# Kernel tuning notes

Hardware: AMD Instinct MI355X
Metric: run time of the kernel (lower is better)

## Reference

```python
import jax, jax.numpy as jnp
import numpy as np

N = 100_000      # nodes
F_IN = 256       # num_features
HID = 128        # args.hidden
C = 32           # num_classes
E = 1_600_000    # edges
EPS = 0.1        # AntiSymmetricConv epsilon
GAMMA = 0.1      # AntiSymmetricConv gamma


def setup_inputs() -> dict:
    key = jax.random.key(0)
    ks = jax.random.split(key, 10)
    def rn(k, shape, scale=0.05):
        return jax.random.normal(k, shape, dtype=jnp.float32) * scale
    x = jax.random.normal(ks[0], (N, F_IN), dtype=jnp.float32)
    edge_index = jax.random.randint(ks[1], (2, E), 0, N, dtype=jnp.int32)
    return {
        "x": x,
        "lin1_w": rn(ks[2], (HID, F_IN)), "lin1_b": jnp.zeros((HID,), jnp.float32),
        "lin2_w": rn(ks[3], (C, HID)),   "lin2_b": jnp.zeros((C,), jnp.float32),
        "W1": rn(ks[4], (HID, HID)), "phi1_w": rn(ks[5], (HID, HID)), "b1": jnp.zeros((HID,), jnp.float32),
        "W2": rn(ks[6], (C, C)),     "phi2_w": rn(ks[7], (C, C)),     "b2": jnp.zeros((C,), jnp.float32),
        "edge_index": edge_index,
    }


def gcn_norm(edge_index, n):
    # GCNConv default: add self-loops, symmetric D^-1/2 (A+I) D^-1/2 normalization
    loops = jnp.arange(n, dtype=edge_index.dtype)
    row = jnp.concatenate([edge_index[0], loops])  # source
    col = jnp.concatenate([edge_index[1], loops])  # target (aggregation)
    deg = jax.ops.segment_sum(jnp.ones(row.shape[0], jnp.float32), col, num_segments=n)
    dinv = jnp.where(deg > 0, jax.lax.rsqrt(deg), 0.0)
    return row, col, dinv[row] * dinv[col]


def gcn_conv(x, phi_w, row, col, norm):
    xw = x @ phi_w.T                                  # [N, d]
    msgs = norm[:, None] * xw[row]                    # [E+N, d] gather
    return jax.ops.segment_sum(msgs, col, num_segments=x.shape[0])  # scatter-add


def anti_symmetric_conv(x, row, col, norm, W, phi_w, b):
    d = W.shape[0]
    aw = W - W.T - GAMMA * jnp.eye(d, dtype=W.dtype)  # antisymmetric weight
    h = gcn_conv(x, phi_w, row, col, norm)            # phi(x, edge_index)
    h = jnp.tanh(x @ aw.T + h + b)
    return x + EPS * h                                # one Euler step (num_iters=1)


def reference(x, lin1_w, lin1_b, lin2_w, lin2_b, W1, phi1_w, b1, W2, phi2_w, b2, edge_index):
    row, col, norm = gcn_norm(edge_index, x.shape[0])
    h = jax.nn.relu(x @ lin1_w.T + lin1_b)            # dropout is identity in eval
    h = anti_symmetric_conv(h, row, col, norm, W1, phi1_w, b1)
    h = h @ lin2_w.T + lin2_b
    h = anti_symmetric_conv(h, row, col, norm, W2, phi2_w, b2)
    return jax.nn.log_softmax(h, axis=1)
```

## Files before the change

### kernel.cpp

```cpp
#include <hip/hip_runtime.h>
#include <hip/hip_bf16.h>
#include <math.h>

#define N_NODES 100000
#define F_IN    256
#define HID     128
#define NCLS    32
#define NEDGES  1600000
#define EPS_C   0.1f
#define GAMMA_C 0.1f

#define NBK   782
#define CHUNK 4096
#define NCH   391
#define BMAX  4096

typedef __attribute__((ext_vector_type(8))) short short8;
typedef __attribute__((ext_vector_type(4))) float floatx4;

__device__ __forceinline__ float bf2f(unsigned short u) {
    union { unsigned int u; float f; } c;
    c.u = ((unsigned int)u) << 16;
    return c.f;
}
__device__ __forceinline__ unsigned short f2bf(float f) {
    union { float f; unsigned int u; } c; c.f = f;
    unsigned int u = c.u;
    u += 0x7FFFu + ((u >> 16) & 1u);
    return (unsigned short)(u >> 16);
}

__device__ __forceinline__ short8 cvt8(float4 u, float4 v) {
    short8 r;
    r[0] = (short)f2bf(u.x); r[1] = (short)f2bf(u.y);
    r[2] = (short)f2bf(u.z); r[3] = (short)f2bf(u.w);
    r[4] = (short)f2bf(v.x); r[5] = (short)f2bf(v.y);
    r[6] = (short)f2bf(v.z); r[7] = (short)f2bf(v.w);
    return r;
}

__device__ __forceinline__ float ldf(const void* p, size_t i, int md) {
    return md ? ((const float*)p)[i] : bf2f(((const unsigned short*)p)[i]);
}

__global__ void k_detect(const unsigned short* __restrict__ x, int* __restrict__ mode) {
    __shared__ int cnt;
    if (threadIdx.x == 0) cnt = 0;
    __syncthreads();
    float v = fabsf(bf2f(x[2 * threadIdx.x]));
    if (v > 1e4f || !isfinite(v)) atomicAdd(&cnt, 1);
    __syncthreads();
    if (threadIdx.x == 0) *mode = (cnt >= 8) ? 1 : 0;
}

__global__ __launch_bounds__(256) void k_cvtx(const void* __restrict__ x,
                                              unsigned short* __restrict__ xbf,
                                              const int* __restrict__ dmode, int n8) {
    if (!dmode[0]) return;
    const float* xf = (const float*)x;
    int stride = gridDim.x * 256;
    for (int i = blockIdx.x * 256 + threadIdx.x; i < n8; i += stride) {
        const float* q = xf + (size_t)i * 8;
        float4 u = *(const float4*)q, v = *(const float4*)(q + 4);
        *(short8*)(xbf + (size_t)i * 8) = cvt8(u, v);
    }
}

__global__ __launch_bounds__(256) void k_cvtw(const void* __restrict__ w1,
                                              const void* __restrict__ w2,
                                              const void* __restrict__ w3,
                                              const void* __restrict__ w4,
                                              unsigned short* __restrict__ out,
                                              const int* __restrict__ dmode) {
    if (!dmode[0]) return;
    int i = blockIdx.x * 256 + threadIdx.x;
    const float* src; int off;
    if (i < 4096)      { src = (const float*)w1; off = i; }
    else if (i < 6144) { src = (const float*)w2; off = i - 4096; }
    else if (i < 6656) { src = (const float*)w3; off = i - 6144; }
    else if (i < 6784) { src = (const float*)w4; off = i - 6656; }
    else return;
    const float* q = src + (size_t)off * 8;
    *(short8*)(out + (size_t)i * 8) = cvt8(*(const float4*)q, *(const float4*)(q + 4));
}

__global__ __launch_bounds__(256) void k_hist2(const int* __restrict__ ecol,
                                               int* __restrict__ hist, int e) {
    __shared__ int lh[NBK];
    for (int i = threadIdx.x; i < NBK; i += 256) lh[i] = 0;
    __syncthreads();
    int base = blockIdx.x * CHUNK;
    int lim = base + CHUNK; if (lim > e) lim = e;
    for (int i = base + threadIdx.x; i < lim; i += 256)
        atomicAdd(&lh[ecol[i] >> 7], 1);
    __syncthreads();
    for (int i = threadIdx.x; i < NBK; i += 256) hist[blockIdx.x * NBK + i] = lh[i];
}

__global__ __launch_bounds__(256) void k_tot(const int* __restrict__ hist, int* __restrict__ tot) {
    __shared__ int s[256];
    int b = blockIdx.x;
    int v = 0;
    for (int blk = threadIdx.x; blk < NCH; blk += 256) v += hist[blk * NBK + b];
    s[threadIdx.x] = v;
    __syncthreads();
#pragma unroll
    for (int off = 128; off > 0; off >>= 1) {
        if (threadIdx.x < off) s[threadIdx.x] += s[threadIdx.x + off];
        __syncthreads();
    }
    if (threadIdx.x == 0) tot[b] = s[0];
}

__global__ void k_bscan(const int* __restrict__ tot, int* __restrict__ bbase) {
    __shared__ int s[1024];
    int v = (threadIdx.x < NBK) ? tot[threadIdx.x] : 0;
    s[threadIdx.x] = v;
    __syncthreads();
#pragma unroll
    for (int off = 1; off < 1024; off <<= 1) {
        int t = (threadIdx.x >= off) ? s[threadIdx.x - off] : 0;
        __syncthreads();
        s[threadIdx.x] += t;
        __syncthreads();
    }
    if (threadIdx.x < NBK) bbase[threadIdx.x] = s[threadIdx.x] - v;
}

__global__ __launch_bounds__(512) void k_colscan(const int* __restrict__ hist,
                                                 const int* __restrict__ bbase,
                                                 int* __restrict__ off) {
    __shared__ int s[512];
    int b = blockIdx.x, t = threadIdx.x;
    int v = (t < NCH) ? hist[t * NBK + b] : 0;
    s[t] = v;
    __syncthreads();
#pragma unroll
    for (int o = 1; o < 512; o <<= 1) {
        int u = (t >= o) ? s[t - o] : 0;
        __syncthreads();
        s[t] += u;
        __syncthreads();
    }
    if (t < NCH) off[t * NBK + b] = s[t] - v + bbase[b];
}

__global__ __launch_bounds__(256) void k_pass3(
    const int* __restrict__ erow, const int* __restrict__ ecol,
    const int* __restrict__ off, unsigned int* __restrict__ pairs, int e)
{
    __shared__ int lh[NBK];
    __shared__ int lex[NBK + 1];
    __shared__ int cur[NBK];
    __shared__ int wsum[256];
    __shared__ unsigned int sp[CHUNK];
    int base = blockIdx.x * CHUNK;
    int lim = base + CHUNK; if (lim > e) lim = e;
    int cnt = lim - base;

    for (int i = threadIdx.x; i < NBK; i += 256) lh[i] = 0;
    __syncthreads();
    for (int i = base + threadIdx.x; i < lim; i += 256)
        atomicAdd(&lh[ecol[i] >> 7], 1);
    __syncthreads();

    int t4 = threadIdx.x * 4;
    int a0 = (t4 + 0 < NBK) ? lh[t4 + 0] : 0;
    int a1 = (t4 + 1 < NBK) ? lh[t4 + 1] : 0;
    int a2 = (t4 + 2 < NBK) ? lh[t4 + 2] : 0;
    int a3 = (t4 + 3 < NBK) ? lh[t4 + 3] : 0;
    int mysum = a0 + a1 + a2 + a3;
    wsum[threadIdx.x] = mysum;
    __syncthreads();
#pragma unroll
    for (int o = 1; o < 256; o <<= 1) {
        int u = (threadIdx.x >= o) ? wsum[threadIdx.x - o] : 0;
        __syncthreads();
        wsum[threadIdx.x] += u;
        __syncthreads();
    }
    int run = wsum[threadIdx.x] - mysum;
    if (t4 + 0 < NBK) { lex[t4 + 0] = run;            cur[t4 + 0] = run; }
    if (t4 + 1 < NBK) { lex[t4 + 1] = run + a0;       cur[t4 + 1] = run + a0; }
    if (t4 + 2 < NBK) { lex[t4 + 2] = run + a0 + a1;  cur[t4 + 2] = run + a0 + a1; }
    if (t4 + 3 < NBK) { lex[t4 + 3] = run + a0 + a1 + a2; cur[t4 + 3] = run + a0 + a1 + a2; }
    if (threadIdx.x == 0) lex[NBK] = cnt;
    __syncthreads();

    for (int i = base + threadIdx.x; i < lim; i += 256) {
        int dst = ecol[i], src = erow[i];
        int b = dst >> 7;
        int p = atomicAdd(&cur[b], 1);
        sp[p] = ((unsigned int)src << 7) | (unsigned int)(dst & 127);
    }
    __syncthreads();

    for (int i = threadIdx.x; i < cnt; i += 256) {
        int loB = 0, hiB = NBK;
        while (hiB - loB > 1) {
            int mid = (loB + hiB) >> 1;
            if (lex[mid] <= i) loB = mid; else hiB = mid;
        }
        pairs[off[blockIdx.x * NBK + loB] + (i - lex[loB])] = sp[i];
    }
}

__global__ __launch_bounds__(256) void k_build(
    const int* __restrict__ tot, const int* __restrict__ bbase,
    const unsigned int* __restrict__ pairs,
    int* __restrict__ srt, int* __restrict__ row_start, int* __restrict__ cend,
    float* __restrict__ dinv, int n)
{
    __shared__ int lh[128];
    __shared__ int lo[128];
    __shared__ unsigned int se[BMAX];
    int b = blockIdx.x;
    int nb = tot[b]; if (nb > BMAX) nb = BMAX;
    int base = bbase[b];
    if (threadIdx.x < 128) lh[threadIdx.x] = 0;
    __syncthreads();
    for (int e = threadIdx.x; e < nb; e += 256) {
        unsigned int pk = pairs[(size_t)base + e];
        se[e] = pk;
        atomicAdd(&lh[pk & 127u], 1);
    }
    __syncthreads();
    if (threadIdx.x < 128) lo[threadIdx.x] = lh[threadIdx.x];
    __syncthreads();
#pragma unroll
    for (int off = 1; off < 128; off <<= 1) {
        int t = (threadIdx.x < 128 && threadIdx.x >= off) ? lo[threadIdx.x - off] : 0;
        __syncthreads();
        if (threadIdx.x < 128) lo[threadIdx.x] += t;
        __syncthreads();
    }
    int node = b * 128 + threadIdx.x;
    if (threadIdx.x < 128 && node < n) {
        int inc = lo[threadIdx.x], cnt = lh[threadIdx.x];
        row_start[node] = base + inc - cnt;
        cend[node]      = base + inc;
        dinv[node]      = rsqrtf((float)cnt + 1.0f);
    }
    __syncthreads();
    if (threadIdx.x < 128) lh[threadIdx.x] = lo[threadIdx.x] - lh[threadIdx.x];
    __syncthreads();
    for (int e = threadIdx.x; e < nb; e += 256) {
        unsigned int pk = se[e];
        int pos = atomicAdd(&lh[pk & 127u], 1);
        srt[base + pos] = (int)(pk >> 7);
    }
}

__global__ void k_aw(const void* __restrict__ W, unsigned short* __restrict__ aw,
                     const int* __restrict__ dmode, int d) {
    int idx = blockIdx.x * blockDim.x + threadIdx.x;
    if (idx >= d * d) return;
    int md = dmode[0];
    int n = idx / d, k = idx - n * d;
    float v = ldf(W, n * d + k, md) - ldf(W, k * d + n, md) - ((n == k) ? GAMMA_C : 0.0f);
    aw[idx] = f2bf(v);
}

template<int K, int NCB, int NCF, int EPI, int NSPLIT, bool ASEL, bool BSEL>
__global__ __launch_bounds__(512) void k_gemm6(
    const void* A, const unsigned short* Acvt,
    const void* B, const unsigned short* Bcvt, const void* bias,
    unsigned short* Cout,
    const unsigned short* agg, const unsigned short* xw, const float* dinv,
    const int* dmode, void* opout, int M)
{
    constexpr int KP = K + 8;
    constexpr int NT = NCB / 16;
    constexpr int KS = K / 32;
    constexpr int SN = (NCB * K) / 4096;
    __shared__ __align__(16) unsigned short sB[NCB * KP];
    const int md = dmode[0];

    const unsigned short* Ab = (ASEL && md) ? Acvt : (const unsigned short*)A;
    const unsigned short* Bb = (BSEL && md) ? Bcvt : (const unsigned short*)B;

    const int rowblk = (NSPLIT > 1) ? ((int)blockIdx.x / NSPLIT) : (int)blockIdx.x;
    const int col0   = (NSPLIT > 1) ? ((int)blockIdx.x % NSPLIT) * NCB : 0;

    const int lane = threadIdx.x & 63;
    const int wave = threadIdx.x >> 6;
    const int l15  = lane & 15;
    const int quad = lane >> 4;
    const int row0 = rowblk * 128 + wave * 16;

    int ar = row0 + l15;
    int am = ar < M ? ar : M - 1;

    short8 a[KS];
#pragma unroll
    for (int s = 0; s < KS; ++s)
        a[s] = *(const short8*)(Ab + (size_t)am * K + s * 32 + quad * 8);

    if constexpr (SN >= 1) {
        short8 st[SN];
#pragma unroll
        for (int i = 0; i < SN; ++i) {
            int base = threadIdx.x * 8 + i * 4096;
            int r = base / K, c = base % K;
            st[i] = *(const short8*)(Bb + (size_t)(col0 + r) * K + c);
        }
#pragma unroll
        for (int i = 0; i < SN; ++i) {
            int base = threadIdx.x * 8 + i * 4096;
            int r = base / K, c = base % K;
            *(short8*)(sB + r * KP + c) = st[i];
        }
    } else {
        if (threadIdx.x < (NCB * K) / 8) {
            int base = threadIdx.x * 8;
            int r = base / K, c = base % K;
            *(short8*)(sB + r * KP + c) =
                *(const short8*)(Bb + (size_t)(col0 + r) * K + c);
        }
    }
    __builtin_amdgcn_sched_barrier(0);
    __syncthreads();

    floatx4 acc[NT];
#pragma unroll
    for (int t = 0; t < NT; ++t) acc[t] = (floatx4){0.f, 0.f, 0.f, 0.f};

#pragma unroll
    for (int s = 0; s < KS; ++s) {
        short8 b[NT];
#pragma unroll
        for (int t = 0; t < NT; ++t)
            b[t] = *(const short8*)(sB + (t * 16 + l15) * KP + s * 32 + quad * 8);
#pragma unroll
        for (int t = 0; t < NT; ++t)
            acc[t] = __builtin_amdgcn_mfma_f32_16x16x32_bf16(a[s], b[t], acc[t], 0, 0, 0);
    }

    const unsigned short* Ares = Ab;
#pragma unroll
    for (int reg = 0; reg < 4; ++reg) {
        int rr = row0 + quad * 4 + reg;
        if (EPI == 4) {
            int rrc = rr < M ? rr : M - 1;
            float dv = dinv[rrc];
            float val[NT];
#pragma unroll
            for (int t = 0; t < NT; ++t) {
                int col = t * 16 + l15;
                float z = acc[t][reg]
                        + bf2f(agg[(size_t)rrc * NCF + col])
                        + dv * bf2f(xw[(size_t)rrc * NCF + col])
                        + ldf(bias, col, md);
                val[t] = bf2f(Ares[(size_t)rrc * K + col]) + EPS_C * tanhf(z);
            }
            float m = val[0];
#pragma unroll
            for (int t = 1; t < NT; ++t) m = fmaxf(m, val[t]);
#pragma unroll
            for (int msk = 1; msk < 16; msk <<= 1) m = fmaxf(m, __shfl_xor(m, msk));
            float s = 0.f;
#pragma unroll
            for (int t = 0; t < NT; ++t) s += expf(val[t] - m);
#pragma unroll
            for (int msk = 1; msk < 16; msk <<= 1) s += __shfl_xor(s, msk);
            float ls = m + logf(s);
            if (rr < M) {
#pragma unroll
                for (int t = 0; t < NT; ++t) {
                    int col = t * 16 + l15;
                    float r = val[t] - ls;
                    if (md) ((float*)opout)[(size_t)rr * NCF + col] = r;
                    else    ((unsigned short*)opout)[(size_t)rr * NCF + col] = f2bf(r);
                }
            }
        } else {
            if (rr >= M) continue;
#pragma unroll
            for (int t = 0; t < NT; ++t) {
                int gcol = col0 + t * 16 + l15;
                float v = acc[t][reg];
                if (EPI == 0) { v += ldf(bias, gcol, md); v = v > 0.f ? v : 0.f; }
                else if (EPI == 5) { v *= dinv[rr]; }
                else if (EPI == 3) {
                    float dv = dinv[rr];
                    float z = v + bf2f(agg[(size_t)rr * NCF + gcol])
                            + dv * bf2f(xw[(size_t)rr * NCF + gcol])
                            + ldf(bias, gcol, md);
                    v = bf2f(Ares[(size_t)rr * K + gcol]) + EPS_C * tanhf(z);
                }
                Cout[(size_t)rr * NCF + gcol] = f2bf(v);
            }
        }
    }
}

__global__ __launch_bounds__(256) void k_lin2phi2(
    const unsigned short* __restrict__ A,
    const void* __restrict__ B1, const unsigned short* __restrict__ B1c,
    const void* __restrict__ bias,
    const void* __restrict__ B2, const unsigned short* __restrict__ B2c,
    unsigned short* __restrict__ h3, unsigned short* __restrict__ xws2,
    const float* __restrict__ dinv, const int* __restrict__ dmode, int M)
{
    constexpr int K1 = 128, KP1 = 136, KP2 = 40;
    __shared__ __align__(16) unsigned short sB1[32 * KP1];
    __shared__ __align__(16) unsigned short sB2[32 * KP2];
    __shared__ __align__(16) unsigned short sT[128 * KP2];
    const int md = dmode[0];

    const unsigned short* B1b = md ? B1c : (const unsigned short*)B1;
    const unsigned short* B2b = md ? B2c : (const unsigned short*)B2;

    const int lane = threadIdx.x & 63;
    const int wave = threadIdx.x >> 6;
    const int l15  = lane & 15;
    const int quad = lane >> 4;
    const int row0 = blockIdx.x * 128 + wave * 32;

    int am[2];
#pragma unroll
    for (int rt = 0; rt < 2; ++rt) {
        int r = row0 + rt * 16 + l15;
        am[rt] = r < M ? r : M - 1;
    }

    short8 a1[4][2];
#pragma unroll
    for (int s = 0; s < 4; ++s)
#pragma unroll
        for (int rt = 0; rt < 2; ++rt)
            a1[s][rt] = *(const short8*)(A + (size_t)am[rt] * K1 + s * 32 + quad * 8);

    short8 s1[2], s2;
    const bool has2 = threadIdx.x * 8 < 1024;
#pragma unroll
    for (int i = 0; i < 2; ++i)
        s1[i] = *(const short8*)(B1b + threadIdx.x * 8 + i * 2048);
    if (has2)
        s2 = *(const short8*)(B2b + threadIdx.x * 8);
#pragma unroll
    for (int i = 0; i < 2; ++i) {
        int base = threadIdx.x * 8 + i * 2048;
        int r = base / K1, c = base - r * K1;
        *(short8*)(sB1 + r * KP1 + c) = s1[i];
    }
    if (has2) {
        int base = threadIdx.x * 8;
        int r = base / 32, c = base - r * 32;
        *(short8*)(sB2 + r * KP2 + c) = s2;
    }
    __builtin_amdgcn_sched_barrier(0);
    __syncthreads();

    floatx4 acc[2][2];
#pragma unroll
    for (int rt = 0; rt < 2; ++rt) { acc[rt][0] = (floatx4){0,0,0,0}; acc[rt][1] = (floatx4){0,0,0,0}; }

#pragma unroll
    for (int s = 0; s < 4; ++s) {
#pragma unroll
        for (int rt = 0; rt < 2; ++rt) {
#pragma unroll
            for (int t = 0; t < 2; ++t) {
                short8 b = *(const short8*)(sB1 + (t * 16 + l15) * KP1 + s * 32 + quad * 8);
                acc[rt][t] = __builtin_amdgcn_mfma_f32_16x16x32_bf16(a1[s][rt], b, acc[rt][t], 0, 0, 0);
            }
        }
    }
#pragma unroll
    for (int rt = 0; rt < 2; ++rt)
#pragma unroll
        for (int reg = 0; reg < 4; ++reg) {
            int rr = row0 + rt * 16 + quad * 4 + reg;
            int lr = wave * 32 + rt * 16 + quad * 4 + reg;
#pragma unroll
            for (int t = 0; t < 2; ++t) {
                int col = t * 16 + l15;
                unsigned short hv = f2bf(acc[rt][t][reg] + ldf(bias, col, md));
                sT[lr * KP2 + col] = hv;
                if (rr < M) h3[(size_t)rr * 32 + col] = hv;
            }
        }
    __syncthreads();

    floatx4 a2[2][2];
#pragma unroll
    for (int rt = 0; rt < 2; ++rt) {
        short8 a = *(const short8*)(sT + (wave * 32 + rt * 16 + l15) * KP2 + quad * 8);
#pragma unroll
        for (int t = 0; t < 2; ++t) {
            short8 b = *(const short8*)(sB2 + (t * 16 + l15) * KP2 + quad * 8);
            a2[rt][t] = __builtin_amdgcn_mfma_f32_16x16x32_bf16(a, b, (floatx4){0,0,0,0}, 0, 0, 0);
        }
    }
#pragma unroll
    for (int rt = 0; rt < 2; ++rt)
#pragma unroll
        for (int reg = 0; reg < 4; ++reg) {
            int rr = row0 + rt * 16 + quad * 4 + reg;
            if (rr >= M) continue;
            float dv = dinv[rr];
#pragma unroll
            for (int t = 0; t < 2; ++t)
                xws2[(size_t)rr * 32 + t * 16 + l15] = f2bf(dv * a2[rt][t][reg]);
        }
}

__global__ __launch_bounds__(256) void k_gather128(
    const int* __restrict__ srt, const int* __restrict__ rs,
    const int* __restrict__ cend,
    const unsigned short* __restrict__ xws, const float* __restrict__ dinv,
    unsigned short* __restrict__ agg, int n)
{
    int node = blockIdx.x * 8 + (threadIdx.x >> 5);
    int l = threadIdx.x & 31;
    if (node >= n) return;
    int j = rs[node], end = cend[node];
    float a0 = 0.f, a1 = 0.f, a2 = 0.f, a3 = 0.f;
    int jend = j + ((end - j) & ~7);
    while (j < jend) {
        int idx[8];
#pragma unroll
        for (int k = 0; k < 8; ++k) idx[k] = srt[j + k];
        uint2 p[8];
#pragma unroll
        for (int k = 0; k < 8; ++k)
            p[k] = *(const uint2*)(xws + (size_t)idx[k] * 128 + l * 4);
#pragma unroll
        for (int k = 0; k < 8; ++k) {
            a0 += bf2f((unsigned short)(p[k].x & 0xFFFFu));
            a1 += bf2f((unsigned short)(p[k].x >> 16));
            a2 += bf2f((unsigned short)(p[k].y & 0xFFFFu));
            a3 += bf2f((unsigned short)(p[k].y >> 16));
        }
        j += 8;
    }
    if (j < end) {
        int idx[8];
#pragma unroll
        for (int k = 0; k < 8; ++k) {
            int jj = j + k;
            idx[k] = srt[jj < end ? jj : end - 1];
        }
        uint2 p[8];
#pragma unroll
        for (int k = 0; k < 8; ++k)
            p[k] = *(const uint2*)(xws + (size_t)idx[k] * 128 + l * 4);
#pragma unroll
        for (int k = 0; k < 8; ++k) {
            if (j + k < end) {
                a0 += bf2f((unsigned short)(p[k].x & 0xFFFFu));
                a1 += bf2f((unsigned short)(p[k].x >> 16));
                a2 += bf2f((unsigned short)(p[k].y & 0xFFFFu));
                a3 += bf2f((unsigned short)(p[k].y >> 16));
            }
        }
    }
    float dn = dinv[node];
    uint2 out;
    out.x = (unsigned int)f2bf(dn * a0) | ((unsigned int)f2bf(dn * a1) << 16);
    out.y = (unsigned int)f2bf(dn * a2) | ((unsigned int)f2bf(dn * a3) << 16);
    *(uint2*)(agg + (size_t)node * 128 + l * 4) = out;
}

__global__ __launch_bounds__(256) void k_gather32(
    const int* __restrict__ srt, const int* __restrict__ rs,
    const int* __restrict__ cend,
    const unsigned short* __restrict__ xws, const float* __restrict__ dinv,
    unsigned short* __restrict__ agg, int n)
{
    int node = blockIdx.x * 32 + (threadIdx.x >> 3);
    int l = threadIdx.x & 7;
    if (node >= n) return;
    int j = rs[node], end = cend[node];
    float a0 = 0.f, a1 = 0.f, a2 = 0.f, a3 = 0.f;
    int jend = j + ((end - j) & ~7);
    while (j < jend) {
        int idx[8];
#pragma unroll
        for (int k = 0; k < 8; ++k) idx[k] = srt[j + k];
        uint2 p[8];
#pragma unroll
        for (int k = 0; k < 8; ++k)
            p[k] = *(const uint2*)(xws + (size_t)idx[k] * 32 + l * 4);
#pragma unroll
        for (int k = 0; k < 8; ++k) {
            a0 += bf2f((unsigned short)(p[k].x & 0xFFFFu));
            a1 += bf2f((unsigned short)(p[k].x >> 16));
            a2 += bf2f((unsigned short)(p[k].y & 0xFFFFu));
            a3 += bf2f((unsigned short)(p[k].y >> 16));
        }
        j += 8;
    }
    if (j < end) {
        int idx[8];
#pragma unroll
        for (int k = 0; k < 8; ++k) {
            int jj = j + k;
            idx[k] = srt[jj < end ? jj : end - 1];
        }
        uint2 p[8];
#pragma unroll
        for (int k = 0; k < 8; ++k)
            p[k] = *(const uint2*)(xws + (size_t)idx[k] * 32 + l * 4);
#pragma unroll
        for (int k = 0; k < 8; ++k) {
            if (j + k < end) {
                a0 += bf2f((unsigned short)(p[k].x & 0xFFFFu));
                a1 += bf2f((unsigned short)(p[k].x >> 16));
                a2 += bf2f((unsigned short)(p[k].y & 0xFFFFu));
                a3 += bf2f((unsigned short)(p[k].y >> 16));
            }
        }
    }
    float dn = dinv[node];
    uint2 out;
    out.x = (unsigned int)f2bf(dn * a0) | ((unsigned int)f2bf(dn * a1) << 16);
    out.y = (unsigned int)f2bf(dn * a2) | ((unsigned int)f2bf(dn * a3) << 16);
    *(uint2*)(agg + (size_t)node * 32 + l * 4) = out;
}

extern "C" void kernel_launch(void* const* d_in, const int* in_sizes, int n_in,
                              void* d_out, int out_size, void* d_ws, size_t ws_size,
                              hipStream_t stream)
{
    const void* x      = d_in[0];
    const void* lin1_w = d_in[1];
    const void* lin1_b = d_in[2];
    const void* lin2_w = d_in[3];
    const void* lin2_b = d_in[4];
    const void* W1     = d_in[5];
    const void* phi1w  = d_in[6];
    const void* b1     = d_in[7];
    const void* W2     = d_in[8];
    const void* phi2w  = d_in[9];
    const void* b2     = d_in[10];
    const int* eidx    = (const int*)d_in[11];
    const int* erow = eidx;
    const int* ecol = eidx + NEDGES;

    char* ws = (char*)d_ws;
    float* dinv          = (float*)ws;
    int*   dmode         = (int*)(ws + 400000);
    unsigned short* aw1  = (unsigned short*)(ws + 401408);
    unsigned short* aw2  = (unsigned short*)(ws + 435200);
    int* tot             = (int*)(ws + 440320);
    int* bbase           = (int*)(ws + 443648);
    int* row_start       = (int*)(ws + 446976);
    int* cend            = (int*)(ws + 846976);
    int* srt             = (int*)(ws + 1246976);
    int* hist            = (int*)(ws + 7646976);
    int* offb            = (int*)(ws + 8870912);
    unsigned short* wbf  = (unsigned short*)(ws + 10094080);
    unsigned short* h1   = (unsigned short*)(ws + 10485760);
    unsigned short* xws1 = h1 + (size_t)N_NODES * HID;
    unsigned short* agg1 = xws1 + (size_t)N_NODES * HID;
    unsigned short* h2   = xws1;
    unsigned short* h3   = h1;
    unsigned short* xws2 = agg1;
    unsigned short* agg2 = agg1 + (size_t)N_NODES * NCLS;
    unsigned int* pairs  = (unsigned int*)agg1;
    unsigned short* xbf  = xws1;

    unsigned short* bw1 = wbf;
    unsigned short* bp1 = wbf + 32768;
    unsigned short* bw2 = wbf + 49152;
    unsigned short* bp2 = wbf + 53248;

    const int GB = 256;
    const int NB5 = (N_NODES + 127) / 128;
    k_detect<<<1, 256, 0, stream>>>((const unsigned short*)x, dmode);

    k_hist2<<<NCH, 256, 0, stream>>>(ecol, hist, NEDGES);
    k_tot<<<NBK, 256, 0, stream>>>(hist, tot);
    k_bscan<<<1, 1024, 0, stream>>>(tot, bbase);
    k_colscan<<<NBK, 512, 0, stream>>>(hist, bbase, offb);
    k_pass3<<<NCH, 256, 0, stream>>>(erow, ecol, offb, pairs, NEDGES);
    k_build<<<NBK, 256, 0, stream>>>(tot, bbase, pairs, srt, row_start, cend, dinv, N_NODES);

    k_aw<<<(HID * HID + GB - 1) / GB, GB, 0, stream>>>(W1, aw1, dmode, HID);
    k_aw<<<(NCLS * NCLS + GB - 1) / GB, GB, 0, stream>>>(W2, aw2, dmode, NCLS);
    k_cvtw<<<27, 256, 0, stream>>>(lin1_w, phi1w, lin2_w, phi2w, wbf, dmode);
    k_cvtx<<<2048, 256, 0, stream>>>(x, xbf, dmode, N_NODES * F_IN / 8);

    k_gemm6<256, 64, 128, 0, 2, true, true><<<NB5 * 2, 512, 0, stream>>>(
        x, xbf, lin1_w, bw1, lin1_b, h1, nullptr, nullptr, nullptr, dmode, nullptr, N_NODES);
    k_gemm6<128, 128, 128, 5, 1, false, true><<<NB5, 512, 0, stream>>>(
        h1, nullptr, phi1w, bp1, nullptr, xws1, nullptr, nullptr, dinv, dmode, nullptr, N_NODES);
    k_gather128<<<(N_NODES + 7) / 8, 256, 0, stream>>>(
        srt, row_start, cend, xws1, dinv, agg1, N_NODES);
    k_gemm6<128, 128, 128, 3, 1, false, false><<<NB5, 512, 0, stream>>>(
        h1, nullptr, aw1, nullptr, b1, h2, agg1, xws1, dinv, dmode, nullptr, N_NODES);
    k_lin2phi2<<<(N_NODES + 127) / 128, 256, 0, stream>>>(
        h2, lin2_w, bw2, lin2_b, phi2w, bp2, h3, xws2, dinv, dmode, N_NODES);
    k_gather32<<<(N_NODES + 31) / 32, 256, 0, stream>>>(
        srt, row_start, cend, xws2, dinv, agg2, N_NODES);
    k_gemm6<32, 32, 32, 4, 1, false, false><<<NB5, 512, 0, stream>>>(
        h3, nullptr, aw2, nullptr, b2, nullptr, agg2, xws2, dinv, dmode, d_out, N_NODES);
}
```

Baseline: 427.9 us.

## Sort nodes by degree for gathers, widen gather loads, drop pass3 binary search

Adds a counting sort of nodes by in-degree (histogram, scan, scatter) so that gather kernels process nodes in degree order, which is meant to reduce wavefront divergence from unequal neighbor counts. The gather kernels now use 16-byte loads with 8 elements per lane, halving the lanes per node. k_pass3 stores each edge's bucket id in shared memory instead of binary-searching the bucket for every output element. The change adds four small kernel launches and an extra ord indirection, and output writes become scattered by node order.

```diff
diff --git a/kernel.cpp b/kernel.cpp
--- a/kernel.cpp
+++ b/kernel.cpp
@@ -150,10 +150,11 @@
     const int* __restrict__ off, unsigned int* __restrict__ pairs, int e)
 {
     __shared__ int lh[NBK];
-    __shared__ int lex[NBK + 1];
+    __shared__ int lex[NBK];
     __shared__ int cur[NBK];
     __shared__ int wsum[256];
     __shared__ unsigned int sp[CHUNK];
+    __shared__ unsigned short sbk[CHUNK];
     int base = blockIdx.x * CHUNK;
     int lim = base + CHUNK; if (lim > e) lim = e;
     int cnt = lim - base;
@@ -184,7 +185,6 @@
     if (t4 + 1 < NBK) { lex[t4 + 1] = run + a0;       cur[t4 + 1] = run + a0; }
     if (t4 + 2 < NBK) { lex[t4 + 2] = run + a0 + a1;  cur[t4 + 2] = run + a0 + a1; }
     if (t4 + 3 < NBK) { lex[t4 + 3] = run + a0 + a1 + a2; cur[t4 + 3] = run + a0 + a1 + a2; }
-    if (threadIdx.x == 0) lex[NBK] = cnt;
     __syncthreads();
 
     for (int i = base + threadIdx.x; i < lim; i += 256) {
@@ -192,16 +192,13 @@
         int b = dst >> 7;
         int p = atomicAdd(&cur[b], 1);
         sp[p] = ((unsigned int)src << 7) | (unsigned int)(dst & 127);
+        sbk[p] = (unsigned short)b;
     }
     __syncthreads();
 
     for (int i = threadIdx.x; i < cnt; i += 256) {
-        int loB = 0, hiB = NBK;
-        while (hiB - loB > 1) {
-            int mid = (loB + hiB) >> 1;
-            if (lex[mid] <= i) loB = mid; else hiB = mid;
-        }
-        pairs[off[blockIdx.x * NBK + loB] + (i - lex[loB])] = sp[i];
+        int b = sbk[i];
+        pairs[off[blockIdx.x * NBK + b] + (i - lex[b])] = sp[i];
     }
 }
 
@@ -248,6 +245,43 @@
         unsigned int pk = se[e];
         int pos = atomicAdd(&lh[pk & 127u], 1);
         srt[base + pos] = (int)(pk >> 7);
+    }
+}
+
+__global__ void k_dzero(int* __restrict__ dh) { dh[threadIdx.x] = 0; }
+
+__global__ __launch_bounds__(256) void k_dhist(const int* __restrict__ rs,
+                                               const int* __restrict__ ce,
+                                               int* __restrict__ dh, int n) {
+    __shared__ int lh[64];
+    if (threadIdx.x < 64) lh[threadIdx.x] = 0;
+    __syncthreads();
+    for (int i = blockIdx.x * 256 + threadIdx.x; i < n; i += gridDim.x * 256) {
+        int d = ce[i] - rs[i]; if (d > 63) d = 63;
+        atomicAdd(&lh[d], 1);
+    }
+    __syncthreads();
+    if (threadIdx.x < 64 && lh[threadIdx.x]) atomicAdd(&dh[threadIdx.x], lh[threadIdx.x]);
+}
+
+__global__ void k_dscan(const int* __restrict__ dh, int* __restrict__ dcur) {
+    __shared__ int s[64];
+    int v = dh[threadIdx.x]; s[threadIdx.x] = v; __syncthreads();
+#pragma unroll
+    for (int o = 1; o < 64; o <<= 1) {
+        int t = (threadIdx.x >= o) ? s[threadIdx.x - o] : 0;
+        __syncthreads(); s[threadIdx.x] += t; __syncthreads();
+    }
+    dcur[threadIdx.x] = s[threadIdx.x] - v;
+}
+
+__global__ __launch_bounds__(256) void k_dscat(const int* __restrict__ rs,
+                                               const int* __restrict__ ce,
+                                               int* __restrict__ dcur,
+                                               int* __restrict__ ord, int n) {
+    for (int i = blockIdx.x * 256 + threadIdx.x; i < n; i += gridDim.x * 256) {
+        int d = ce[i] - rs[i]; if (d > 63) d = 63;
+        ord[atomicAdd(&dcur[d], 1)] = i;
     }
 }
 
@@ -508,31 +542,30 @@
 
 __global__ __launch_bounds__(256) void k_gather128(
     const int* __restrict__ srt, const int* __restrict__ rs,
-    const int* __restrict__ cend,
+    const int* __restrict__ cend, const int* __restrict__ ord,
     const unsigned short* __restrict__ xws, const float* __restrict__ dinv,
     unsigned short* __restrict__ agg, int n)
 {
-    int node = blockIdx.x * 8 + (threadIdx.x >> 5);
-    int l = threadIdx.x & 31;
-    if (node >= n) return;
+    int gid = blockIdx.x * 16 + (threadIdx.x >> 4);
+    int l = threadIdx.x & 15;
+    if (gid >= n) return;
+    int node = ord[gid];
     int j = rs[node], end = cend[node];
-    float a0 = 0.f, a1 = 0.f, a2 = 0.f, a3 = 0.f;
+    float ac[8] = {0.f, 0.f, 0.f, 0.f, 0.f, 0.f, 0.f, 0.f};
     int jend = j + ((end - j) & ~7);
     while (j < jend) {
         int idx[8];
 #pragma unroll
         for (int k = 0; k < 8; ++k) idx[k] = srt[j + k];
-        uint2 p[8];
+        short8 p[8];
 #pragma unroll
         for (int k = 0; k < 8; ++k)
-            p[k] = *(const uint2*)(xws + (size_t)idx[k] * 128 + l * 4);
-#pragma unroll
-        for (int k = 0; k < 8; ++k) {
-            a0 += bf2f((unsigned short)(p[k].x & 0xFFFFu));
-            a1 += bf2f((unsigned short)(p[k].x >> 16));
-            a2 += bf2f((unsigned short)(p[k].y & 0xFFFFu));
-            a3 += bf2f((unsigned short)(p[k].y >> 16));
-        }
+            p[k] = *(const short8*)(xws + (size_t)idx[k] * 128 + l * 8);
+#pragma unroll
+        for (int k = 0; k < 8; ++k)
+#pragma unroll
+            for (int e = 0; e < 8; ++e)
+                ac[e] += bf2f((unsigned short)p[k][e]);
         j += 8;
     }
     if (j < end) {
@@ -542,54 +575,52 @@
             int jj = j + k;
             idx[k] = srt[jj < end ? jj : end - 1];
         }
-        uint2 p[8];
+        short8 p[8];
 #pragma unroll
         for (int k = 0; k < 8; ++k)
-            p[k] = *(const uint2*)(xws + (size_t)idx[k] * 128 + l * 4);
+            p[k] = *(const short8*)(xws + (size_t)idx[k] * 128 + l * 8);
 #pragma unroll
         for (int k = 0; k < 8; ++k) {
             if (j + k < end) {
-                a0 += bf2f((unsigned short)(p[k].x & 0xFFFFu));
-                a1 += bf2f((unsigned short)(p[k].x >> 16));
-                a2 += bf2f((unsigned short)(p[k].y & 0xFFFFu));
-                a3 += bf2f((unsigned short)(p[k].y >> 16));
+#pragma unroll
+                for (int e = 0; e < 8; ++e)
+                    ac[e] += bf2f((unsigned short)p[k][e]);
             }
         }
     }
     float dn = dinv[node];
-    uint2 out;
-    out.x = (unsigned int)f2bf(dn * a0) | ((unsigned int)f2bf(dn * a1) << 16);
-    out.y = (unsigned int)f2bf(dn * a2) | ((unsigned int)f2bf(dn * a3) << 16);
-    *(uint2*)(agg + (size_t)node * 128 + l * 4) = out;
+    short8 out;
+#pragma unroll
+    for (int e = 0; e < 8; ++e) out[e] = (short)f2bf(dn * ac[e]);
+    *(short8*)(agg + (size_t)node * 128 + l * 8) = out;
 }
 
 __global__ __launch_bounds__(256) void k_gather32(
     const int* __restrict__ srt, const int* __restrict__ rs,
-    const int* __restrict__ cend,
+    const int* __restrict__ cend, const int* __restrict__ ord,
     const unsigned short* __restrict__ xws, const float* __restrict__ dinv,
     unsigned short* __restrict__ agg, int n)
 {
-    int node = blockIdx.x * 32 + (threadIdx.x >> 3);
-    int l = threadIdx.x & 7;
-    if (node >= n) return;
+    int gid = blockIdx.x * 64 + (threadIdx.x >> 2);
+    int l = threadIdx.x & 3;
+    if (gid >= n) return;
+    int node = ord[gid];
     int j = rs[node], end = cend[node];
-    float a0 = 0.f, a1 = 0.f, a2 = 0.f, a3 = 0.f;
+    float ac[8] = {0.f, 0.f, 0.f, 0.f, 0.f, 0.f, 0.f, 0.f};
     int jend = j + ((end - j) & ~7);
     while (j < jend) {
         int idx[8];
 #pragma unroll
         for (int k = 0; k < 8; ++k) idx[k] = srt[j + k];
-        uint2 p[8];
+        short8 p[8];
 #pragma unroll
         for (int k = 0; k < 8; ++k)
-            p[k] = *(const uint2*)(xws + (size_t)idx[k] * 32 + l * 4);
-#pragma unroll
-        for (int k = 0; k < 8; ++k) {
-            a0 += bf2f((unsigned short)(p[k].x & 0xFFFFu));
-            a1 += bf2f((unsigned short)(p[k].x >> 16));
-            a2 += bf2f((unsigned short)(p[k].y & 0xFFFFu));
-            a3 += bf2f((unsigned short)(p[k].y >> 16));
-        }
+            p[k] = *(const short8*)(xws + (size_t)idx[k] * 32 + l * 8);
+#pragma unroll
+        for (int k = 0; k < 8; ++k)
+#pragma unroll
+            for (int e = 0; e < 8; ++e)
+                ac[e] += bf2f((unsigned short)p[k][e]);
         j += 8;
     }
     if (j < end) {
@@ -599,25 +630,24 @@
             int jj = j + k;
             idx[k] = srt[jj < end ? jj : end - 1];
         }
-        uint2 p[8];
+        short8 p[8];
 #pragma unroll
         for (int k = 0; k < 8; ++k)
-            p[k] = *(const uint2*)(xws + (size_t)idx[k] * 32 + l * 4);
+            p[k] = *(const short8*)(xws + (size_t)idx[k] * 32 + l * 8);
 #pragma unroll
         for (int k = 0; k < 8; ++k) {
             if (j + k < end) {
-                a0 += bf2f((unsigned short)(p[k].x & 0xFFFFu));
-                a1 += bf2f((unsigned short)(p[k].x >> 16));
-                a2 += bf2f((unsigned short)(p[k].y & 0xFFFFu));
-                a3 += bf2f((unsigned short)(p[k].y >> 16));
+#pragma unroll
+                for (int e = 0; e < 8; ++e)
+                    ac[e] += bf2f((unsigned short)p[k][e]);
             }
         }
     }
     float dn = dinv[node];
-    uint2 out;
-    out.x = (unsigned int)f2bf(dn * a0) | ((unsigned int)f2bf(dn * a1) << 16);
-    out.y = (unsigned int)f2bf(dn * a2) | ((unsigned int)f2bf(dn * a3) << 16);
-    *(uint2*)(agg + (size_t)node * 32 + l * 4) = out;
+    short8 out;
+#pragma unroll
+    for (int e = 0; e < 8; ++e) out[e] = (short)f2bf(dn * ac[e]);
+    *(short8*)(agg + (size_t)node * 32 + l * 8) = out;
 }
 
 extern "C" void kernel_launch(void* const* d_in, const int* in_sizes, int n_in,
@@ -661,6 +691,9 @@
     unsigned short* agg2 = agg1 + (size_t)N_NODES * NCLS;
     unsigned int* pairs  = (unsigned int*)agg1;
     unsigned short* xbf  = xws1;
+    int* ord             = (int*)(ws + 87285760);
+    int* dh              = (int*)(ws + 87685760);
+    int* dcur            = dh + 64;
 
     unsigned short* bw1 = wbf;
     unsigned short* bp1 = wbf + 32768;
@@ -678,6 +711,11 @@
     k_pass3<<<NCH, 256, 0, stream>>>(erow, ecol, offb, pairs, NEDGES);
     k_build<<<NBK, 256, 0, stream>>>(tot, bbase, pairs, srt, row_start, cend, dinv, N_NODES);
 
+    k_dzero<<<1, 64, 0, stream>>>(dh);
+    k_dhist<<<98, 256, 0, stream>>>(row_start, cend, dh, N_NODES);
+    k_dscan<<<1, 64, 0, stream>>>(dh, dcur);
+    k_dscat<<<98, 256, 0, stream>>>(row_start, cend, dcur, ord, N_NODES);
+
     k_aw<<<(HID * HID + GB - 1) / GB, GB, 0, stream>>>(W1, aw1, dmode, HID);
     k_aw<<<(NCLS * NCLS + GB - 1) / GB, GB, 0, stream>>>(W2, aw2, dmode, NCLS);
     k_cvtw<<<27, 256, 0, stream>>>(lin1_w, phi1w, lin2_w, phi2w, wbf, dmode);
@@ -687,14 +725,14 @@
         x, xbf, lin1_w, bw1, lin1_b, h1, nullptr, nullptr, nullptr, dmode, nullptr, N_NODES);
     k_gemm6<128, 128, 128, 5, 1, false, true><<<NB5, 512, 0, stream>>>(
         h1, nullptr, phi1w, bp1, nullptr, xws1, nullptr, nullptr, dinv, dmode, nullptr, N_NODES);
-    k_gather128<<<(N_NODES + 7) / 8, 256, 0, stream>>>(
-        srt, row_start, cend, xws1, dinv, agg1, N_NODES);
+    k_gather128<<<(N_NODES + 15) / 16, 256, 0, stream>>>(
+        srt, row_start, cend, ord, xws1, dinv, agg1, N_NODES);
     k_gemm6<128, 128, 128, 3, 1, false, false><<<NB5, 512, 0, stream>>>(
         h1, nullptr, aw1, nullptr, b1, h2, agg1, xws1, dinv, dmode, nullptr, N_NODES);
     k_lin2phi2<<<(N_NODES + 127) / 128, 256, 0, stream>>>(
         h2, lin2_w, bw2, lin2_b, phi2w, bp2, h3, xws2, dinv, dmode, N_NODES);
-    k_gather32<<<(N_NODES + 31) / 32, 256, 0, stream>>>(
-        srt, row_start, cend, xws2, dinv, agg2, N_NODES);
+    k_gather32<<<(N_NODES + 63) / 64, 256, 0, stream>>>(
+        srt, row_start, cend, ord, xws2, dinv, agg2, N_NODES);
     k_gemm6<32, 32, 32, 4, 1, false, false><<<NB5, 512, 0, stream>>>(
         h3, nullptr, aw2, nullptr, b2, nullptr, agg2, xws2, dinv, dmode, d_out, N_NODES);
 }
```

After: 697.8 us. +63.1%, slower.
